# Optimization experiments

Hardware: AMD Instinct MI355X
Metric: run time of the kernel (lower is better)

Reference implementation:

```python
import jax, jax.numpy as jnp
import numpy as np

N, DIM = 100000, 512
HID = DIM // 2


def _mlp(z, W1, b1, W2, b2):
    # shared scorer: [N, dim] -> [N, 1]
    h = jax.nn.relu(z @ W1 + b1)
    return h @ W2 + b2


def setup_inputs() -> dict:
    key = jax.random.key(0)
    k1, k2, k3, k4 = jax.random.split(key, 4)
    s1 = 1.0 / np.sqrt(DIM)
    s2 = 1.0 / np.sqrt(HID)
    return {
        "z1": jax.random.normal(k1, (N, DIM), dtype=jnp.float32),
        "z2": jax.random.normal(k2, (N, DIM), dtype=jnp.float32),
        "W1": jax.random.normal(k3, (DIM, HID), dtype=jnp.float32) * s1,
        "b1": jnp.zeros((HID,), dtype=jnp.float32),
        "W2": jax.random.normal(k4, (HID, 1), dtype=jnp.float32) * s2,
        "b2": jnp.zeros((1,), dtype=jnp.float32),
    }


def reference(z1, z2, W1, b1, W2, b2):
    x = _mlp(z1, W1, b1, W2, b2)  # [N, 1]
    y = _mlp(z2, W1, b1, W2, b2)  # [N, 1]
    # exp-normalize pair: score_x = e^x / (e^x + e^y) == sigmoid(x - y)
    # computed exactly as in the original (plain exp, no max-subtract)
    e_x = jnp.exp(x)
    e_y = jnp.exp(y)
    denom = e_x + e_y
    score_x = e_x / denom  # [N, 1]
    score_y = e_y / denom  # [N, 1]
    # diag(score) @ z  ==  score * z  (row-wise broadcast scale)
    return score_x * z1 + score_y * z2
```

## Files before the change

### kernel.cpp

```cpp
#include <hip/hip_runtime.h>
#include <hip/hip_bf16.h>
#include <cmath>

#define DIM 512
#define HID 256
#define ROWS_PB 32
#define NCHUNK 16
#define CB 16384

typedef __attribute__((ext_vector_type(8))) short short8;
typedef __attribute__((ext_vector_type(4))) float f32x4;
typedef __attribute__((ext_vector_type(4))) unsigned int u32x4;

__device__ __forceinline__ unsigned short f2bf(float f) {
  union { float f; unsigned u; } v; v.f = f;
  unsigned u = v.u;
  return (unsigned short)((u + 0x7FFFu + ((u >> 16) & 1u)) >> 16);
}
__device__ __forceinline__ float bf2f(short h) {
  union { unsigned u; float f; } v;
  v.u = ((unsigned)(unsigned short)h) << 16;
  return v.f;
}

#define LGKM_BAR()                                        \
  do {                                                    \
    asm volatile("s_waitcnt lgkmcnt(0)" ::: "memory");    \
    __builtin_amdgcn_s_barrier();                         \
    __builtin_amdgcn_sched_barrier(0);                    \
  } while (0)

__global__ void w1_swz_kernel(const float* __restrict__ W1,
                              unsigned short* __restrict__ w1s) {
  int tid = blockIdx.x * blockDim.x + threadIdx.x;
  if (tid >= DIM * HID) return;
  int k = tid / HID;
  int c = tid - k * HID;
  w1s[(((k >> 3) * HID) + c) * 8 + (k & 7)] = f2bf(W1[tid]);
}

__device__ __forceinline__ short8 cvt8(const f32x4 p0, const f32x4 p1) {
  short8 r;
  r[0] = (short)f2bf(p0[0]); r[1] = (short)f2bf(p0[1]);
  r[2] = (short)f2bf(p0[2]); r[3] = (short)f2bf(p0[3]);
  r[4] = (short)f2bf(p1[0]); r[5] = (short)f2bf(p1[1]);
  r[6] = (short)f2bf(p1[2]); r[7] = (short)f2bf(p1[3]);
  return r;
}

__device__ __forceinline__ void wcombine(float wa, const short8 a, float wb,
                                         const short8 b, f32x4& o0, f32x4& o1) {
#pragma unroll
  for (int i = 0; i < 4; ++i) {
    o0[i] = wa * bf2f(a[i]) + wb * bf2f(b[i]);
    o1[i] = wa * bf2f(a[i + 4]) + wb * bf2f(b[i + 4]);
  }
}

__global__ __launch_bounds__(256, 2) void fa_main_kernel(
    const float* __restrict__ z1, const float* __restrict__ z2,
    const unsigned short* __restrict__ w1s,
    const float* __restrict__ bias1, const float* __restrict__ W2,
    const float* __restrict__ bias2, float* __restrict__ out, int n) {
  __shared__ char smem[81920];
  short8* Az = (short8*)smem;
  char* Bs = smem + 65536;
  float* xs = (float*)(smem + 65536);

  const int t = threadIdx.x;
  const int w = t >> 6;
  const int l = t & 63;
  const int l15 = l & 15, l16 = l >> 4;
  const int s = w & 1;
  const int tl = w >> 1;
  const int row0 = blockIdx.x * ROWS_PB;
  const int myrow = row0 + tl * 16 + l15;
  const bool rok = myrow < n;
  const float* zz = s ? z2 : z1;
  const float* ap = zz + (size_t)myrow * DIM + (l16 << 3);
  const f32x4 zf4 = (f32x4){0.f, 0.f, 0.f, 0.f};

  u32x4 breg0, breg1, breg2, breg3;
#define BLOAD(c)                                            \
  {                                                         \
    const u32x4* g = (const u32x4*)w1s + (c) * 1024 + t;    \
    breg0 = g[0];                                           \
    breg1 = g[256];                                         \
    breg2 = g[512];                                         \
    breg3 = g[768];                                         \
  }
#define BWRITE()                                            \
  {                                                         \
    u32x4* d = (u32x4*)Bs + t;                              \
    d[0] = breg0;                                           \
    d[256] = breg1;                                         \
    d[512] = breg2;                                         \
    d[768] = breg3;                                         \
  }

  BLOAD(0);
  __builtin_amdgcn_sched_barrier(0);
#pragma unroll
  for (int g = 0; g < 4; ++g) {
    f32x4 p[4][2];
#pragma unroll
    for (int j = 0; j < 4; ++j) {
      const float* pp = ap + (((g << 2) + j) << 5);
      p[j][0] = rok ? *(const f32x4*)(pp) : zf4;
      p[j][1] = rok ? *(const f32x4*)(pp + 4) : zf4;
    }
#pragma unroll
    for (int j = 0; j < 4; ++j)
      Az[((s * NCHUNK + (g << 2) + j) * 2 + tl) * 64 + l] =
          cvt8(p[j][0], p[j][1]);
  }
  BWRITE();
  __syncthreads();

  f32x4 acc[16];
#pragma unroll
  for (int f = 0; f < 16; ++f) acc[f] = zf4;

#pragma unroll
  for (int c = 0; c < NCHUNK; ++c) {
    if (c + 1 < NCHUNK) BLOAD(c + 1);
    __builtin_amdgcn_sched_barrier(0);
    const short8* bp = (const short8*)Bs + (l16 << 8) + l15;
    const short8 af = Az[((s * NCHUNK + c) * 2 + tl) * 64 + l];
    short8 bf[16];
#pragma unroll
    for (int f = 0; f < 16; ++f) bf[f] = bp[f << 4];
    __builtin_amdgcn_sched_barrier(0);
#pragma unroll
    for (int f = 0; f < 16; ++f)
      acc[f] =
          __builtin_amdgcn_mfma_f32_16x16x32_bf16(af, bf[f], acc[f], 0, 0, 0);
    LGKM_BAR();
    if (c + 1 < NCHUNK) BWRITE();
    LGKM_BAR();
  }

  float part[4] = {0.f, 0.f, 0.f, 0.f};
#pragma unroll
  for (int f = 0; f < 16; ++f) {
    const int cc = (f << 4) + l15;
    const float w2v = W2[cc];
    const float b1v = bias1[cc];
#pragma unroll
    for (int r = 0; r < 4; ++r) {
      const float hh = acc[f][r] + b1v;
      part[r] += (hh > 0.f) ? hh * w2v : 0.f;
    }
  }
#pragma unroll
  for (int r = 0; r < 4; ++r) {
#pragma unroll
    for (int m = 1; m < 16; m <<= 1) part[r] += __shfl_xor(part[r], m, 16);
  }
  if (l15 == 0) {
#pragma unroll
    for (int r = 0; r < 4; ++r)
      xs[s * ROWS_PB + tl * 16 + (l16 << 2) + r] = part[r];
  }
  __syncthreads();

  const float x = xs[tl * 16 + l15];
  const float y = xs[ROWS_PB + tl * 16 + l15];
  const float sx = 1.f / (1.f + __expf(y - x));
  const float sy = 1.f - sx;
  float* orow = out + (size_t)myrow * DIM + (l16 << 3);
  if (rok) {
#pragma unroll
    for (int j = 0; j < 8; ++j) {
      const int cc = (s << 3) + j;
      const short8 a0 = Az[((0 * NCHUNK + cc) * 2 + tl) * 64 + l];
      const short8 a1 = Az[((1 * NCHUNK + cc) * 2 + tl) * 64 + l];
      f32x4 o0, o1;
      wcombine(sx, a0, sy, a1, o0, o1);
      *(f32x4*)(orow + (cc << 5)) = o0;
      *(f32x4*)(orow + (cc << 5) + 4) = o1;
    }
  }
#undef BLOAD
#undef BWRITE
}

extern "C" void kernel_launch(void* const* d_in, const int* in_sizes, int n_in,
                              void* d_out, int out_size, void* d_ws,
                              size_t ws_size, hipStream_t stream) {
  const float* z1 = (const float*)d_in[0];
  const float* z2 = (const float*)d_in[1];
  const float* W1 = (const float*)d_in[2];
  const float* b1 = (const float*)d_in[3];
  const float* W2 = (const float*)d_in[4];
  const float* b2 = (const float*)d_in[5];
  float* out = (float*)d_out;
  const int n = in_sizes[0] / DIM;
  unsigned short* w1s = (unsigned short*)d_ws;

  hipLaunchKernelGGL(w1_swz_kernel, dim3((DIM * HID + 255) / 256), dim3(256),
                     0, stream, W1, w1s);
  const int nwg = (n + ROWS_PB - 1) / ROWS_PB;
  hipLaunchKernelGGL(fa_main_kernel, dim3(nwg), dim3(256), 0, stream, z1, z2,
                     w1s, b1, W2, b2, out, n);
}
```

Measured before the change: 187.3 us.

## Stream activation loads through the K loop with two-deep register prefetch

The kernel used to load and convert every activation chunk into LDS before the MFMA loop started. Now it loads two chunks ahead into registers, then converts and stores each chunk to LDS inside the loop while the next chunk is fetched. This lets global loads of z overlap the MFMA work instead of stalling in the prologue. The cost is extra live registers, and the order in which chunks are issued changes.

```diff
diff --git a/kernel.cpp b/kernel.cpp
--- a/kernel.cpp
+++ b/kernel.cpp
@@ -99,21 +99,11 @@
   }
 
   BLOAD(0);
-  __builtin_amdgcn_sched_barrier(0);
-#pragma unroll
-  for (int g = 0; g < 4; ++g) {
-    f32x4 p[4][2];
-#pragma unroll
-    for (int j = 0; j < 4; ++j) {
-      const float* pp = ap + (((g << 2) + j) << 5);
-      p[j][0] = rok ? *(const f32x4*)(pp) : zf4;
-      p[j][1] = rok ? *(const f32x4*)(pp + 4) : zf4;
-    }
-#pragma unroll
-    for (int j = 0; j < 4; ++j)
-      Az[((s * NCHUNK + (g << 2) + j) * 2 + tl) * 64 + l] =
-          cvt8(p[j][0], p[j][1]);
-  }
+  f32x4 paA0, paA1, paB0, paB1;
+  paA0 = rok ? *(const f32x4*)(ap) : zf4;
+  paA1 = rok ? *(const f32x4*)(ap + 4) : zf4;
+  paB0 = rok ? *(const f32x4*)(ap + 32) : zf4;
+  paB1 = rok ? *(const f32x4*)(ap + 36) : zf4;
   BWRITE();
   __syncthreads();
 
@@ -124,9 +114,24 @@
 #pragma unroll
   for (int c = 0; c < NCHUNK; ++c) {
     if (c + 1 < NCHUNK) BLOAD(c + 1);
+    short8 af;
+    if (c & 1)
+      af = cvt8(paB0, paB1);
+    else
+      af = cvt8(paA0, paA1);
+    Az[((s * NCHUNK + c) * 2 + tl) * 64 + l] = af;
+    if (c + 2 < NCHUNK) {
+      const float* apn = ap + ((c + 2) << 5);
+      if (c & 1) {
+        paB0 = rok ? *(const f32x4*)(apn) : zf4;
+        paB1 = rok ? *(const f32x4*)(apn + 4) : zf4;
+      } else {
+        paA0 = rok ? *(const f32x4*)(apn) : zf4;
+        paA1 = rok ? *(const f32x4*)(apn + 4) : zf4;
+      }
+    }
     __builtin_amdgcn_sched_barrier(0);
     const short8* bp = (const short8*)Bs + (l16 << 8) + l15;
-    const short8 af = Az[((s * NCHUNK + c) * 2 + tl) * 64 + l];
     short8 bf[16];
 #pragma unroll
     for (int f = 0; f < 16; ++f) bf[f] = bp[f << 4];
```

After: 184.4 us, median of 2. Within noise of the previous version (-1.5%).

## Stream A operands from registers, double-buffer W1 in LDS, re-read z for output

Applied to the files above, without the earlier changes.

The kernel no longer stages the whole bf16 copy of z1/z2 in LDS. A fragments are prefetched two steps ahead into registers and converted on the fly, and W1 chunks are doubled in size and double-buffered in LDS, which cuts one barrier per step. The final combine re-reads z1 and z2 from global memory in fp32 with coalesced row-wise loads, rather than using the bf16 LDS copy. This shrinks LDS use and improves output precision, but it adds an extra global read of both inputs (likely served by L2/MALL) and more register pressure.

```diff
diff --git a/kernel.cpp b/kernel.cpp
--- a/kernel.cpp
+++ b/kernel.cpp
@@ -5,8 +5,8 @@
 #define DIM 512
 #define HID 256
 #define ROWS_PB 32
-#define NCHUNK 16
-#define CB 16384
+#define NSTEP 8
+#define SB 32768
 
 typedef __attribute__((ext_vector_type(8))) short short8;
 typedef __attribute__((ext_vector_type(4))) float f32x4;
@@ -16,11 +16,6 @@
   union { float f; unsigned u; } v; v.f = f;
   unsigned u = v.u;
   return (unsigned short)((u + 0x7FFFu + ((u >> 16) & 1u)) >> 16);
-}
-__device__ __forceinline__ float bf2f(short h) {
-  union { unsigned u; float f; } v;
-  v.u = ((unsigned)(unsigned short)h) << 16;
-  return v.f;
 }
 
 #define LGKM_BAR()                                        \
@@ -48,24 +43,13 @@
   return r;
 }
 
-__device__ __forceinline__ void wcombine(float wa, const short8 a, float wb,
-                                         const short8 b, f32x4& o0, f32x4& o1) {
-#pragma unroll
-  for (int i = 0; i < 4; ++i) {
-    o0[i] = wa * bf2f(a[i]) + wb * bf2f(b[i]);
-    o1[i] = wa * bf2f(a[i + 4]) + wb * bf2f(b[i + 4]);
-  }
-}
-
 __global__ __launch_bounds__(256, 2) void fa_main_kernel(
     const float* __restrict__ z1, const float* __restrict__ z2,
     const unsigned short* __restrict__ w1s,
     const float* __restrict__ bias1, const float* __restrict__ W2,
     const float* __restrict__ bias2, float* __restrict__ out, int n) {
-  __shared__ char smem[81920];
-  short8* Az = (short8*)smem;
-  char* Bs = smem + 65536;
-  float* xs = (float*)(smem + 65536);
+  __shared__ char smem[2 * SB + 256];
+  float* xs = (float*)(smem + 2 * SB);
 
   const int t = threadIdx.x;
   const int w = t >> 6;
@@ -80,41 +64,34 @@
   const float* ap = zz + (size_t)myrow * DIM + (l16 << 3);
   const f32x4 zf4 = (f32x4){0.f, 0.f, 0.f, 0.f};
 
-  u32x4 breg0, breg1, breg2, breg3;
-#define BLOAD(c)                                            \
+  u32x4 br0, br1, br2, br3, br4, br5, br6, br7;
+#define BLOAD(i)                                            \
   {                                                         \
-    const u32x4* g = (const u32x4*)w1s + (c) * 1024 + t;    \
-    breg0 = g[0];                                           \
-    breg1 = g[256];                                         \
-    breg2 = g[512];                                         \
-    breg3 = g[768];                                         \
-  }
-#define BWRITE()                                            \
+    const u32x4* g = (const u32x4*)w1s + (i) * 2048 + t;    \
+    br0 = g[0];    br1 = g[256];  br2 = g[512];  br3 = g[768]; \
+    br4 = g[1024]; br5 = g[1280]; br6 = g[1536]; br7 = g[1792]; \
+  }
+#define BWRITE(buf)                                         \
   {                                                         \
-    u32x4* d = (u32x4*)Bs + t;                              \
-    d[0] = breg0;                                           \
-    d[256] = breg1;                                         \
-    d[512] = breg2;                                         \
-    d[768] = breg3;                                         \
+    u32x4* d = (u32x4*)(smem + (buf) * SB) + t;             \
+    d[0] = br0;    d[256] = br1;  d[512] = br2;  d[768] = br3; \
+    d[1024] = br4; d[1280] = br5; d[1536] = br6; d[1792] = br7; \
+  }
+
+  f32x4 sA[4], sB[4];
+#define ALOAD(i, slot)                                      \
+  {                                                         \
+    const float* p = ap + ((i) << 6);                       \
+    slot[0] = rok ? *(const f32x4*)(p) : zf4;               \
+    slot[1] = rok ? *(const f32x4*)(p + 4) : zf4;           \
+    slot[2] = rok ? *(const f32x4*)(p + 32) : zf4;          \
+    slot[3] = rok ? *(const f32x4*)(p + 36) : zf4;          \
   }
 
   BLOAD(0);
-  __builtin_amdgcn_sched_barrier(0);
-#pragma unroll
-  for (int g = 0; g < 4; ++g) {
-    f32x4 p[4][2];
-#pragma unroll
-    for (int j = 0; j < 4; ++j) {
-      const float* pp = ap + (((g << 2) + j) << 5);
-      p[j][0] = rok ? *(const f32x4*)(pp) : zf4;
-      p[j][1] = rok ? *(const f32x4*)(pp + 4) : zf4;
-    }
-#pragma unroll
-    for (int j = 0; j < 4; ++j)
-      Az[((s * NCHUNK + (g << 2) + j) * 2 + tl) * 64 + l] =
-          cvt8(p[j][0], p[j][1]);
-  }
-  BWRITE();
+  ALOAD(0, sA);
+  ALOAD(1, sB);
+  BWRITE(0);
   __syncthreads();
 
   f32x4 acc[16];
@@ -122,21 +99,32 @@
   for (int f = 0; f < 16; ++f) acc[f] = zf4;
 
 #pragma unroll
-  for (int c = 0; c < NCHUNK; ++c) {
-    if (c + 1 < NCHUNK) BLOAD(c + 1);
+  for (int i = 0; i < NSTEP; ++i) {
+    if (i + 1 < NSTEP) BLOAD(i + 1);
+    short8 af0, af1;
+    if (i & 1) {
+      af0 = cvt8(sB[0], sB[1]);
+      af1 = cvt8(sB[2], sB[3]);
+    } else {
+      af0 = cvt8(sA[0], sA[1]);
+      af1 = cvt8(sA[2], sA[3]);
+    }
+    if (i + 2 < NSTEP) {
+      if (i & 1) ALOAD(i + 2, sB) else ALOAD(i + 2, sA);
+    }
     __builtin_amdgcn_sched_barrier(0);
-    const short8* bp = (const short8*)Bs + (l16 << 8) + l15;
-    const short8 af = Az[((s * NCHUNK + c) * 2 + tl) * 64 + l];
-    short8 bf[16];
-#pragma unroll
-    for (int f = 0; f < 16; ++f) bf[f] = bp[f << 4];
-    __builtin_amdgcn_sched_barrier(0);
+    const short8* bp0 =
+        (const short8*)(smem + (i & 1) * SB) + (l16 << 8) + l15;
+    const short8* bp1 = bp0 + 1024;
 #pragma unroll
     for (int f = 0; f < 16; ++f)
-      acc[f] =
-          __builtin_amdgcn_mfma_f32_16x16x32_bf16(af, bf[f], acc[f], 0, 0, 0);
-    LGKM_BAR();
-    if (c + 1 < NCHUNK) BWRITE();
+      acc[f] = __builtin_amdgcn_mfma_f32_16x16x32_bf16(af0, bp0[f << 4],
+                                                       acc[f], 0, 0, 0);
+#pragma unroll
+    for (int f = 0; f < 16; ++f)
+      acc[f] = __builtin_amdgcn_mfma_f32_16x16x32_bf16(af1, bp1[f << 4],
+                                                       acc[f], 0, 0, 0);
+    if (i + 1 < NSTEP) BWRITE((i + 1) & 1);
     LGKM_BAR();
   }
 
@@ -164,25 +152,33 @@
   }
   __syncthreads();
 
-  const float x = xs[tl * 16 + l15];
-  const float y = xs[ROWS_PB + tl * 16 + l15];
-  const float sx = 1.f / (1.f + __expf(y - x));
-  const float sy = 1.f - sx;
-  float* orow = out + (size_t)myrow * DIM + (l16 << 3);
-  if (rok) {
-#pragma unroll
-    for (int j = 0; j < 8; ++j) {
-      const int cc = (s << 3) + j;
-      const short8 a0 = Az[((0 * NCHUNK + cc) * 2 + tl) * 64 + l];
-      const short8 a1 = Az[((1 * NCHUNK + cc) * 2 + tl) * 64 + l];
-      f32x4 o0, o1;
-      wcombine(sx, a0, sy, a1, o0, o1);
-      *(f32x4*)(orow + (cc << 5)) = o0;
-      *(f32x4*)(orow + (cc << 5) + 4) = o1;
+#pragma unroll
+  for (int j = 0; j < 8; ++j) {
+    const int rl = (w << 3) + j;
+    const int grow = row0 + rl;
+    if (grow < n) {
+      const float x = xs[rl];
+      const float y = xs[ROWS_PB + rl];
+      const float sx = 1.f / (1.f + __expf(y - x));
+      const float sy = 1.f - sx;
+      const size_t off = (size_t)grow * DIM + (l << 2);
+#pragma unroll
+      for (int half = 0; half < 2; ++half) {
+        const size_t o = off + (half << 8);
+        const f32x4 a4 = *(const f32x4*)(z1 + o);
+        const f32x4 b4 = *(const f32x4*)(z2 + o);
+        f32x4 ov;
+        ov[0] = sx * a4[0] + sy * b4[0];
+        ov[1] = sx * a4[1] + sy * b4[1];
+        ov[2] = sx * a4[2] + sy * b4[2];
+        ov[3] = sx * a4[3] + sy * b4[3];
+        *(f32x4*)(out + o) = ov;
+      }
     }
   }
 #undef BLOAD
 #undef BWRITE
+#undef ALOAD
 }
 
 extern "C" void kernel_launch(void* const* d_in, const int* in_sizes, int n_in,
```

After: 197.8 us. +5.6%, slower.
